# Optimization experiments

Hardware: AMD Instinct MI355X
Metric: run time of the kernel (lower is better)

## Reference

```python
import jax, jax.numpy as jnp
import numpy as np

B, D, H, W, C = 2, 128, 128, 128, 8
GD = GH = GW = 96


def setup_inputs() -> dict:
    key = jax.random.key(0)
    k1, k2 = jax.random.split(key)
    inputs = jax.random.normal(k1, (B, D, H, W, C), dtype=jnp.float32)
    # sample_coords uniform over the valid voxel range [0, size-1] per spatial dim
    sizes = jnp.array([D - 1, H - 1, W - 1], dtype=jnp.float32)
    sample_coords = jax.random.uniform(k2, (B, GD, GH, GW, 3), dtype=jnp.float32) * sizes
    return {"inputs": inputs, "sample_coords": sample_coords}


def reference(inputs, sample_coords):
    # Trilinear resampling with REPLICATE boundary (clamp), matching
    # ResamplerLayer.resample_linear + boundary_replicate.
    input_size = inputs.shape[1:-1]                       # (D, H, W)
    rank = len(input_size)                                # 3
    floor_c = jnp.floor(sample_coords)                    # [B, gd, gh, gw, 3]
    w = sample_coords - floor_c                           # fractional weights
    wc = 1.0 - w
    i0 = floor_c.astype(jnp.int32)
    c0 = [jnp.clip(i0[..., d], 0, input_size[d] - 1) for d in range(rank)]
    c1 = [jnp.clip(i0[..., d] + 1, 0, input_size[d] - 1) for d in range(rank)]

    bsz = sample_coords.shape[0]
    batch_idx = jnp.arange(bsz).reshape((bsz,) + (1,) * (sample_coords.ndim - 2))

    # Sum over the 2^rank corners; identical math to the recursive
    # pyramid_combination in the original (fixed small unrolled loop).
    out = jnp.zeros(sample_coords.shape[:-1] + (inputs.shape[-1],), inputs.dtype)
    for code in range(2 ** rank):
        bits = [(code >> (rank - 1 - d)) & 1 for d in range(rank)]
        idx = [c1[d] if bits[d] else c0[d] for d in range(rank)]
        samp = inputs[batch_idx, idx[0], idx[1], idx[2]]  # [B, gd, gh, gw, C]
        wt = jnp.ones(sample_coords.shape[:-1], inputs.dtype)
        for d in range(rank):
            wt = wt * (w[..., d] if bits[d] else wc[..., d])
        out = out + samp * wt[..., None]
    return out
```

## Files before the change

kernel.cpp:

```cpp
#include <hip/hip_runtime.h>
#include <stdint.h>


constexpr int B  = 2;
constexpr int D  = 128;
constexpr int H  = 128;
constexpr int W  = 128;
constexpr int C  = 8;
constexpr int GD = 96;
constexpr int GH = 96;
constexpr int GW = 96;
constexpr long long PTS_PER_B = (long long)GD * GH * GW;
constexpr long long NPTS      = (long long)B * PTS_PER_B;
constexpr int NPTS_I = (int)NPTS;

constexpr int TPZ = 16, TPY = 16, TPX = 8;
constexpr int NT_PER_B = TPZ * TPY * TPX;
constexpr int NT = B * NT_PER_B;

constexpr int RZ = 9, RY = 9, RX = 17;
constexpr int RVOX = RZ * RY * RX;

constexpr int TPB_BIN = 1024;
constexpr int PPT     = 8;
constexpr int NB_BIN  = NPTS_I / (TPB_BIN * PPT);
static_assert(NB_BIN * TPB_BIN * PPT == NPTS_I, "exact tiling");
constexpr int BPT = NT / TPB_BIN;

__device__ __forceinline__ int clampi(int v, int lo, int hi) {
    return min(max(v, lo), hi);
}

__device__ __forceinline__ unsigned long long
pack_rec(int i, float zc, float yc, float xc, int b, int& tk)
{
    const int z0 = clampi((int)floorf(zc), 0, D - 1);
    const int y0 = clampi((int)floorf(yc), 0, H - 1);
    const int x0 = clampi((int)floorf(xc), 0, W - 1);
    const int tz = z0 >> 3, ty = y0 >> 3, tx = x0 >> 4;
    tk = (b << 11) | (tz << 7) | (ty << 3) | tx;
    const int qz = clampi((int)((zc - (float)(tz << 3)) * 1024.0f + 0.5f), 0,  8191);
    const int qy = clampi((int)((yc - (float)(ty << 3)) * 1024.0f + 0.5f), 0,  8191);
    const int qx = clampi((int)((xc - (float)(tx << 4)) * 1024.0f + 0.5f), 0, 16383);
    return (unsigned long long)(uint32_t)i
         | ((unsigned long long)qx << 21)
         | ((unsigned long long)qy << 35)
         | ((unsigned long long)qz << 48);
}

__device__ __forceinline__ int tile_of(int b, float zc, float yc, float xc) {
    int z0 = clampi((int)floorf(zc), 0, D - 1);
    int y0 = clampi((int)floorf(yc), 0, H - 1);
    int x0 = clampi((int)floorf(xc), 0, W - 1);
    return (b << 11) | ((z0 >> 3) << 7) | ((y0 >> 3) << 3) | (x0 >> 4);
}

__device__ __forceinline__ uint32_t bf16_rne(float f) {
    uint32_t u = __float_as_uint(f);
    u += 0x7FFFu + ((u >> 16) & 1u);
    return u >> 16;
}
__device__ __forceinline__ uint32_t pack_bf16(float lo, float hi) {
    return bf16_rne(lo) | (bf16_rne(hi) << 16);
}

__global__ __launch_bounds__(TPB_BIN)
void k_hist(const float* __restrict__ coords, uint16_t* __restrict__ blockHist)
{
    __shared__ uint32_t h[NT];
    const int t = threadIdx.x;
#pragma unroll
    for (int j = 0; j < BPT; ++j) h[t + j * TPB_BIN] = 0u;
    __syncthreads();

    const int base = blockIdx.x * (TPB_BIN * PPT);
#pragma unroll
    for (int k = 0; k < PPT; ++k) {
        const int i = base + k * TPB_BIN + t;
        const float zc = coords[3 * i + 0];
        const float yc = coords[3 * i + 1];
        const float xc = coords[3 * i + 2];
        const int b = (i >= (int)PTS_PER_B) ? 1 : 0;
        atomicAdd(&h[tile_of(b, zc, yc, xc)], 1u);
    }
    __syncthreads();
#pragma unroll
    for (int j = 0; j < BPT; ++j) {
        const int c = t + j * TPB_BIN;
        blockHist[blockIdx.x * NT + c] = (uint16_t)h[c];
    }
}

__global__ __launch_bounds__(128)
void k_scan_cols(uint16_t* __restrict__ blockHist, uint32_t* __restrict__ bucketTot)
{
    const int c = blockIdx.x * 128 + threadIdx.x;
    uint32_t acc = 0u;
#pragma unroll 8
    for (int r = 0; r < NB_BIN; ++r) {
        const int o = r * NT + c;
        const uint32_t v = blockHist[o];
        blockHist[o] = (uint16_t)acc;
        acc += v;
    }
    bucketTot[c] = acc;
}

__global__ __launch_bounds__(TPB_BIN)
void k_scan_base(const uint32_t* __restrict__ bucketTot, uint32_t* __restrict__ bucketBase)
{
    __shared__ uint32_t ss[TPB_BIN];
    const int t = threadIdx.x;

    uint32_t l[BPT];
    uint32_t ls = 0u;
#pragma unroll
    for (int j = 0; j < BPT; ++j) {
        l[j] = bucketTot[t * BPT + j];
        ls += l[j];
    }
    ss[t] = ls;
    __syncthreads();
    for (int off = 1; off < TPB_BIN; off <<= 1) {
        const uint32_t v = (t >= off) ? ss[t - off] : 0u;
        __syncthreads();
        ss[t] += v;
        __syncthreads();
    }
    uint32_t basev = ss[t] - ls;
#pragma unroll
    for (int j = 0; j < BPT; ++j) {
        bucketBase[t * BPT + j] = basev;
        basev += l[j];
    }
    if (t == TPB_BIN - 1) bucketBase[NT] = (uint32_t)NPTS_I;
}

__global__ __launch_bounds__(TPB_BIN)
void k_scatter(const float* __restrict__ coords,
               const uint16_t* __restrict__ blockHist,
               const uint32_t* __restrict__ bucketBase,
               unsigned long long* __restrict__ records)
{
    __shared__ uint32_t cur[NT];
    const int t = threadIdx.x;
#pragma unroll
    for (int j = 0; j < BPT; ++j) {
        const int c = t + j * TPB_BIN;
        cur[c] = (uint32_t)blockHist[blockIdx.x * NT + c] + bucketBase[c];
    }
    __syncthreads();

    const int base = blockIdx.x * (TPB_BIN * PPT);
#pragma unroll
    for (int k = 0; k < PPT; ++k) {
        const int i = base + k * TPB_BIN + t;
        const float zc = coords[3 * i + 0];
        const float yc = coords[3 * i + 1];
        const float xc = coords[3 * i + 2];
        const int b = (i >= (int)PTS_PER_B) ? 1 : 0;
        int tk;
        const unsigned long long r = pack_rec(i, zc, yc, xc, b, tk);
        const uint32_t slot = atomicAdd(&cur[tk], 1u);
        records[slot] = r;
    }
}

__device__ __forceinline__ void
process_rec(unsigned long long r, const uint4* __restrict__ tb,
            float* __restrict__ out)
{
    const int idx = (int)(r & 0x1FFFFFull);
    const int qx  = (int)((r >> 21) & 0x3FFFull);
    const int qy  = (int)((r >> 35) & 0x1FFFull);
    const int qz  = (int)((r >> 48) & 0x1FFFull);
    const int lx = qx >> 10, ly = qy >> 10, lz = qz >> 10;
    const float wx1 = (float)(qx & 1023) * (1.0f / 1024.0f), wx0 = 1.0f - wx1;
    const float wy1 = (float)(qy & 1023) * (1.0f / 1024.0f), wy0 = 1.0f - wy1;
    const float wz1 = (float)(qz & 1023) * (1.0f / 1024.0f), wz0 = 1.0f - wz1;

    const int vi = (lz * RY + ly) * RX + lx;

    float a0 = 0.f, a1 = 0.f, a2 = 0.f, a3 = 0.f;
    float a4 = 0.f, a5 = 0.f, a6 = 0.f, a7 = 0.f;
    const float wzs[2] = {wz0, wz1};
    const float wys[2] = {wy0, wy1};
    const float wxs[2] = {wx0, wx1};

#pragma unroll
    for (int iz = 0; iz < 2; ++iz) {
#pragma unroll
        for (int iy = 0; iy < 2; ++iy) {
#pragma unroll
            for (int ix = 0; ix < 2; ++ix) {
                const float wt = wzs[iz] * wys[iy] * wxs[ix];
                const int cv = vi + (iz * RY + iy) * RX + ix;
                const uint4 rv = tb[cv];
                a0 += wt * __uint_as_float(rv.x << 16);
                a1 += wt * __uint_as_float(rv.x & 0xFFFF0000u);
                a2 += wt * __uint_as_float(rv.y << 16);
                a3 += wt * __uint_as_float(rv.y & 0xFFFF0000u);
                a4 += wt * __uint_as_float(rv.z << 16);
                a5 += wt * __uint_as_float(rv.z & 0xFFFF0000u);
                a6 += wt * __uint_as_float(rv.w << 16);
                a7 += wt * __uint_as_float(rv.w & 0xFFFF0000u);
            }
        }
    }

    float* o = out + (long long)idx * C;
    *reinterpret_cast<float4*>(o)     = make_float4(a0, a1, a2, a3);
    *reinterpret_cast<float4*>(o + 4) = make_float4(a4, a5, a6, a7);
}

__global__ __launch_bounds__(256)
void k_sample_tiled(const float* __restrict__ inp,
                    const unsigned long long* __restrict__ records,
                    const uint32_t* __restrict__ bucketBase,
                    float* __restrict__ out)
{
    __shared__ uint4 tile[RVOX];
    const int t = threadIdx.x;

    const int g = blockIdx.x;
    const int c = (g & 7) * (NT >> 3) + (g >> 3);

    const int tx = c & 7;
    const int ty = (c >> 3) & 15;
    const int tz = (c >> 7) & 15;
    const int b  = c >> 11;
    const int z0r = tz << 3, y0r = ty << 3, x0r = tx << 4;

    const uint32_t s = bucketBase[c];
    const uint32_t e = bucketBase[c + 1];
    const bool v0 = (s + (uint32_t)t        < e);
    const bool v1 = (s + (uint32_t)t + 256u < e);
    unsigned long long r0 = 0ull, r1 = 0ull;
    if (v0) r0 = records[s + (uint32_t)t];
    if (v1) r1 = records[s + (uint32_t)t + 256u];

#pragma unroll
    for (int half = 0; half < 2; ++half) {
        float4 a0[3], a1[3];
#pragma unroll
        for (int j = 0; j < 3; ++j) {
            const int v = t + (half * 3 + j) * 256;
            if (v < RVOX) {
                const int lz = v / (RY * RX);
                const int rr = v - lz * (RY * RX);
                const int ly = rr / RX;
                const int lx = rr - ly * RX;
                const int gz = min(z0r + lz, D - 1);
                const int gy = min(y0r + ly, H - 1);
                const int gx = min(x0r + lx, W - 1);
                const int a = ((((b << 7) | gz) << 7 | gy) << 7 | gx) * C;
                a0[j] = *reinterpret_cast<const float4*>(inp + a);
                a1[j] = *reinterpret_cast<const float4*>(inp + a + 4);
            }
        }
#pragma unroll
        for (int j = 0; j < 3; ++j) {
            const int v = t + (half * 3 + j) * 256;
            if (v < RVOX) {
                uint4 pk;
                pk.x = pack_bf16(a0[j].x, a0[j].y);
                pk.y = pack_bf16(a0[j].z, a0[j].w);
                pk.z = pack_bf16(a1[j].x, a1[j].y);
                pk.w = pack_bf16(a1[j].z, a1[j].w);
                tile[v] = pk;
            }
        }
    }
    __syncthreads();

    if (v0) process_rec(r0, tile, out);
    if (v1) process_rec(r1, tile, out);
    for (uint32_t i = s + (uint32_t)t + 512u; i < e; i += 256u)
        process_rec(records[i], tile, out);
}

__global__ __launch_bounds__(256)
void resample_direct(const float* __restrict__ inp,
                     const float* __restrict__ coords,
                     float* __restrict__ out)
{
    const long long i = (long long)blockIdx.x * blockDim.x + threadIdx.x;
    if (i >= NPTS) return;
    const int b = (i >= PTS_PER_B) ? 1 : 0;
    const float zc = coords[3 * i + 0];
    const float yc = coords[3 * i + 1];
    const float xc = coords[3 * i + 2];
    const float fz = floorf(zc), fy = floorf(yc), fx = floorf(xc);
    const float wz1 = zc - fz, wz0 = 1.0f - wz1;
    const float wy1 = yc - fy, wy0 = 1.0f - wy1;
    const float wx1 = xc - fx, wx0 = 1.0f - wx1;
    const int z0 = clampi((int)fz, 0, D - 1);
    const int y0 = clampi((int)fy, 0, H - 1);
    const int x0 = clampi((int)fx, 0, W - 1);
    const int z1 = min(z0 + 1, D - 1);
    const int y1 = min(y0 + 1, H - 1);
    const int x1 = min(x0 + 1, W - 1);
    float4 acc_lo = make_float4(0.f, 0.f, 0.f, 0.f);
    float4 acc_hi = make_float4(0.f, 0.f, 0.f, 0.f);
    const int   zs[2]  = {z0, z1};
    const int   ys[2]  = {y0, y1};
    const int   xs[2]  = {x0, x1};
    const float wzs[2] = {wz0, wz1};
    const float wys[2] = {wy0, wy1};
    const float wxs[2] = {wx0, wx1};
#pragma unroll
    for (int iz = 0; iz < 2; ++iz)
#pragma unroll
        for (int iy = 0; iy < 2; ++iy)
#pragma unroll
            for (int ix = 0; ix < 2; ++ix) {
                const float wt = wzs[iz] * wys[iy] * wxs[ix];
                const int base = ((((b << 7) | zs[iz]) << 7 | ys[iy]) << 7 | xs[ix]) * C;
                const float4 v0 = *reinterpret_cast<const float4*>(inp + base);
                const float4 v1 = *reinterpret_cast<const float4*>(inp + base + 4);
                acc_lo.x += wt * v0.x;  acc_lo.y += wt * v0.y;
                acc_lo.z += wt * v0.z;  acc_lo.w += wt * v0.w;
                acc_hi.x += wt * v1.x;  acc_hi.y += wt * v1.y;
                acc_hi.z += wt * v1.z;  acc_hi.w += wt * v1.w;
            }
    float* o = out + i * C;
    *reinterpret_cast<float4*>(o)     = acc_lo;
    *reinterpret_cast<float4*>(o + 4) = acc_hi;
}

extern "C" void kernel_launch(void* const* d_in, const int* in_sizes, int n_in,
                              void* d_out, int out_size, void* d_ws, size_t ws_size,
                              hipStream_t stream)
{
    const float* inp    = (const float*)d_in[0];
    const float* coords = (const float*)d_in[1];
    float* out          = (float*)d_out;

    const size_t rec_bytes  = (size_t)NPTS_I * sizeof(unsigned long long);
    const size_t hist_bytes = (size_t)NB_BIN * NT * sizeof(uint16_t);
    const size_t base_bytes = (size_t)(NT + 1) * sizeof(uint32_t);
    const size_t tot_bytes  = (size_t)NT * sizeof(uint32_t);
    const size_t needed     = rec_bytes + hist_bytes + base_bytes + tot_bytes;

    if (ws_size < needed) {
        const int nblk = (NPTS_I + 255) / 256;
        resample_direct<<<nblk, 256, 0, stream>>>(inp, coords, out);
        return;
    }

    unsigned long long* records = (unsigned long long*)d_ws;
    uint16_t* blockHist  = (uint16_t*)((char*)d_ws + rec_bytes);
    uint32_t* bucketBase = (uint32_t*)((char*)d_ws + rec_bytes + hist_bytes);
    uint32_t* bucketTot  = (uint32_t*)((char*)d_ws + rec_bytes + hist_bytes + base_bytes);

    k_hist        <<<NB_BIN,   TPB_BIN, 0, stream>>>(coords, blockHist);
    k_scan_cols   <<<NT / 128, 128,     0, stream>>>(blockHist, bucketTot);
    k_scan_base   <<<1,        TPB_BIN, 0, stream>>>(bucketTot, bucketBase);
    k_scatter     <<<NB_BIN,   TPB_BIN, 0, stream>>>(coords, blockHist, bucketBase, records);
    k_sample_tiled<<<NT,       256,     0, stream>>>(inp, records, bucketBase, out);
}
```

Before: 86.96 us.

## Shrink LDS tile z-halo to 8 slices, fetch upper-z corners from global

The shared-memory tile drops its ninth z-slice, so each block stages 8x9x17 voxels instead of 9x9x17. Samples whose upper z corner falls outside the tile (lz==7 in non-top tiles) read those four corners straight from global memory in fp32. The aim is less staging traffic and LDS footprint per block, which may raise occupancy. The cost is divergent global gathers for about one eighth of the samples, and those corners now use fp32 instead of bf16 values.

```diff
diff --git a/kernel.cpp b/kernel.cpp
--- a/kernel.cpp
+++ b/kernel.cpp
@@ -18,8 +18,8 @@
 constexpr int NT_PER_B = TPZ * TPY * TPX;
 constexpr int NT = B * NT_PER_B;
 
-constexpr int RZ = 9, RY = 9, RX = 17;
-constexpr int RVOX = RZ * RY * RX;
+constexpr int SRZ = 8, RY = 9, RX = 17;
+constexpr int RVOX = SRZ * RY * RX;
 
 constexpr int TPB_BIN = 1024;
 constexpr int PPT     = 8;
@@ -166,53 +166,6 @@
     }
 }
 
-__device__ __forceinline__ void
-process_rec(unsigned long long r, const uint4* __restrict__ tb,
-            float* __restrict__ out)
-{
-    const int idx = (int)(r & 0x1FFFFFull);
-    const int qx  = (int)((r >> 21) & 0x3FFFull);
-    const int qy  = (int)((r >> 35) & 0x1FFFull);
-    const int qz  = (int)((r >> 48) & 0x1FFFull);
-    const int lx = qx >> 10, ly = qy >> 10, lz = qz >> 10;
-    const float wx1 = (float)(qx & 1023) * (1.0f / 1024.0f), wx0 = 1.0f - wx1;
-    const float wy1 = (float)(qy & 1023) * (1.0f / 1024.0f), wy0 = 1.0f - wy1;
-    const float wz1 = (float)(qz & 1023) * (1.0f / 1024.0f), wz0 = 1.0f - wz1;
-
-    const int vi = (lz * RY + ly) * RX + lx;
-
-    float a0 = 0.f, a1 = 0.f, a2 = 0.f, a3 = 0.f;
-    float a4 = 0.f, a5 = 0.f, a6 = 0.f, a7 = 0.f;
-    const float wzs[2] = {wz0, wz1};
-    const float wys[2] = {wy0, wy1};
-    const float wxs[2] = {wx0, wx1};
-
-#pragma unroll
-    for (int iz = 0; iz < 2; ++iz) {
-#pragma unroll
-        for (int iy = 0; iy < 2; ++iy) {
-#pragma unroll
-            for (int ix = 0; ix < 2; ++ix) {
-                const float wt = wzs[iz] * wys[iy] * wxs[ix];
-                const int cv = vi + (iz * RY + iy) * RX + ix;
-                const uint4 rv = tb[cv];
-                a0 += wt * __uint_as_float(rv.x << 16);
-                a1 += wt * __uint_as_float(rv.x & 0xFFFF0000u);
-                a2 += wt * __uint_as_float(rv.y << 16);
-                a3 += wt * __uint_as_float(rv.y & 0xFFFF0000u);
-                a4 += wt * __uint_as_float(rv.z << 16);
-                a5 += wt * __uint_as_float(rv.z & 0xFFFF0000u);
-                a6 += wt * __uint_as_float(rv.w << 16);
-                a7 += wt * __uint_as_float(rv.w & 0xFFFF0000u);
-            }
-        }
-    }
-
-    float* o = out + (long long)idx * C;
-    *reinterpret_cast<float4*>(o)     = make_float4(a0, a1, a2, a3);
-    *reinterpret_cast<float4*>(o + 4) = make_float4(a4, a5, a6, a7);
-}
-
 __global__ __launch_bounds__(256)
 void k_sample_tiled(const float* __restrict__ inp,
                     const unsigned long long* __restrict__ records,
@@ -230,53 +183,143 @@
     const int tz = (c >> 7) & 15;
     const int b  = c >> 11;
     const int z0r = tz << 3, y0r = ty << 3, x0r = tx << 4;
+    const bool top_tile = (tz == 15);
+    const int zpart = ((b << 7) | (z0r + 8)) << 14;
 
     const uint32_t s = bucketBase[c];
     const uint32_t e = bucketBase[c + 1];
-    const bool v0 = (s + (uint32_t)t        < e);
-    const bool v1 = (s + (uint32_t)t + 256u < e);
+    const bool rv0 = (s + (uint32_t)t        < e);
+    const bool rv1 = (s + (uint32_t)t + 256u < e);
     unsigned long long r0 = 0ull, r1 = 0ull;
-    if (v0) r0 = records[s + (uint32_t)t];
-    if (v1) r1 = records[s + (uint32_t)t + 256u];
-
-#pragma unroll
-    for (int half = 0; half < 2; ++half) {
+    if (rv0) r0 = records[s + (uint32_t)t];
+    if (rv1) r1 = records[s + (uint32_t)t + 256u];
+
+    {
         float4 a0[3], a1[3];
 #pragma unroll
         for (int j = 0; j < 3; ++j) {
-            const int v = t + (half * 3 + j) * 256;
+            const int v = t + j * 256;
+            const int lz = v / (RY * RX);
+            const int rr = v - lz * (RY * RX);
+            const int ly = rr / RX;
+            const int lx = rr - ly * RX;
+            const int gy = min(y0r + ly, H - 1);
+            const int gx = min(x0r + lx, W - 1);
+            const int a = ((((b << 7) | (z0r + lz)) << 7 | gy) << 7 | gx) * C;
+            a0[j] = *reinterpret_cast<const float4*>(inp + a);
+            a1[j] = *reinterpret_cast<const float4*>(inp + a + 4);
+        }
+#pragma unroll
+        for (int j = 0; j < 3; ++j) {
+            const int v = t + j * 256;
+            uint4 pk;
+            pk.x = pack_bf16(a0[j].x, a0[j].y);
+            pk.y = pack_bf16(a0[j].z, a0[j].w);
+            pk.z = pack_bf16(a1[j].x, a1[j].y);
+            pk.w = pack_bf16(a1[j].z, a1[j].w);
+            tile[v] = pk;
+        }
+#pragma unroll
+        for (int j = 3; j < 5; ++j) {
+            const int v = t + j * 256;
             if (v < RVOX) {
                 const int lz = v / (RY * RX);
                 const int rr = v - lz * (RY * RX);
                 const int ly = rr / RX;
                 const int lx = rr - ly * RX;
-                const int gz = min(z0r + lz, D - 1);
                 const int gy = min(y0r + ly, H - 1);
                 const int gx = min(x0r + lx, W - 1);
-                const int a = ((((b << 7) | gz) << 7 | gy) << 7 | gx) * C;
-                a0[j] = *reinterpret_cast<const float4*>(inp + a);
-                a1[j] = *reinterpret_cast<const float4*>(inp + a + 4);
+                const int a = ((((b << 7) | (z0r + lz)) << 7 | gy) << 7 | gx) * C;
+                a0[j - 3] = *reinterpret_cast<const float4*>(inp + a);
+                a1[j - 3] = *reinterpret_cast<const float4*>(inp + a + 4);
             }
         }
 #pragma unroll
-        for (int j = 0; j < 3; ++j) {
-            const int v = t + (half * 3 + j) * 256;
+        for (int j = 3; j < 5; ++j) {
+            const int v = t + j * 256;
             if (v < RVOX) {
                 uint4 pk;
-                pk.x = pack_bf16(a0[j].x, a0[j].y);
-                pk.y = pack_bf16(a0[j].z, a0[j].w);
-                pk.z = pack_bf16(a1[j].x, a1[j].y);
-                pk.w = pack_bf16(a1[j].z, a1[j].w);
+                pk.x = pack_bf16(a0[j - 3].x, a0[j - 3].y);
+                pk.y = pack_bf16(a0[j - 3].z, a0[j - 3].w);
+                pk.z = pack_bf16(a1[j - 3].x, a1[j - 3].y);
+                pk.w = pack_bf16(a1[j - 3].z, a1[j - 3].w);
                 tile[v] = pk;
             }
         }
     }
     __syncthreads();
 
-    if (v0) process_rec(r0, tile, out);
-    if (v1) process_rec(r1, tile, out);
+    auto sample = [&](unsigned long long r) {
+        const int idx = (int)(r & 0x1FFFFFull);
+        const int qx  = (int)((r >> 21) & 0x3FFFull);
+        const int qy  = (int)((r >> 35) & 0x1FFFull);
+        const int qz  = (int)((r >> 48) & 0x1FFFull);
+        const int lx = qx >> 10, ly = qy >> 10, lz = qz >> 10;
+        const float wx1 = (float)(qx & 1023) * (1.0f / 1024.0f), wx0 = 1.0f - wx1;
+        const float wy1 = (float)(qy & 1023) * (1.0f / 1024.0f), wy0 = 1.0f - wy1;
+        const float wz1 = (float)(qz & 1023) * (1.0f / 1024.0f), wz0 = 1.0f - wz1;
+
+        const float wys[2] = {wy0, wy1};
+        const float wxs[2] = {wx0, wx1};
+
+        float a0 = 0.f, a1 = 0.f, a2 = 0.f, a3 = 0.f;
+        float a4 = 0.f, a5 = 0.f, a6 = 0.f, a7 = 0.f;
+
+        auto lds_corner = [&](int cv, float wt) {
+            const uint4 rv = tile[cv];
+            a0 += wt * __uint_as_float(rv.x << 16);
+            a1 += wt * __uint_as_float(rv.x & 0xFFFF0000u);
+            a2 += wt * __uint_as_float(rv.y << 16);
+            a3 += wt * __uint_as_float(rv.y & 0xFFFF0000u);
+            a4 += wt * __uint_as_float(rv.z << 16);
+            a5 += wt * __uint_as_float(rv.z & 0xFFFF0000u);
+            a6 += wt * __uint_as_float(rv.w << 16);
+            a7 += wt * __uint_as_float(rv.w & 0xFFFF0000u);
+        };
+
+        const int vlo = (lz * RY + ly) * RX + lx;
+#pragma unroll
+        for (int iy = 0; iy < 2; ++iy)
+#pragma unroll
+            for (int ix = 0; ix < 2; ++ix)
+                lds_corner(vlo + iy * RX + ix, wz0 * wys[iy] * wxs[ix]);
+
+        const int zhi = (lz < 7) ? (lz + 1) : (top_tile ? 7 : -1);
+        if (zhi >= 0) {
+            const int vhi = (zhi * RY + ly) * RX + lx;
+#pragma unroll
+            for (int iy = 0; iy < 2; ++iy)
+#pragma unroll
+                for (int ix = 0; ix < 2; ++ix)
+                    lds_corner(vhi + iy * RX + ix, wz1 * wys[iy] * wxs[ix]);
+        } else {
+#pragma unroll
+            for (int iy = 0; iy < 2; ++iy) {
+#pragma unroll
+                for (int ix = 0; ix < 2; ++ix) {
+                    const float wt = wz1 * wys[iy] * wxs[ix];
+                    const int gy = min(y0r + ly + iy, H - 1);
+                    const int gx = min(x0r + lx + ix, W - 1);
+                    const int a = (zpart | (gy << 7) | gx) * C;
+                    const float4 v0 = *reinterpret_cast<const float4*>(inp + a);
+                    const float4 v1 = *reinterpret_cast<const float4*>(inp + a + 4);
+                    a0 += wt * v0.x;  a1 += wt * v0.y;
+                    a2 += wt * v0.z;  a3 += wt * v0.w;
+                    a4 += wt * v1.x;  a5 += wt * v1.y;
+                    a6 += wt * v1.z;  a7 += wt * v1.w;
+                }
+            }
+        }
+
+        float* o = out + (long long)idx * C;
+        *reinterpret_cast<float4*>(o)     = make_float4(a0, a1, a2, a3);
+        *reinterpret_cast<float4*>(o + 4) = make_float4(a4, a5, a6, a7);
+    };
+
+    if (rv0) sample(r0);
+    if (rv1) sample(r1);
     for (uint32_t i = s + (uint32_t)t + 512u; i < e; i += 256u)
-        process_rec(records[i], tile, out);
+        sample(records[i]);
 }
 
 __global__ __launch_bounds__(256)
```

New measurement: 87.49 us. About the same (+0.6%).

## Shrink sampling tiles to 4x8x8 and give each wavefront its own tile

Applied to the files above, without the earlier changes.

Binning tiles shrink from 8x8x16 to 4x8x8 voxels, which quadruples the number of buckets. The sampling kernel now assigns one tile per 64-lane wavefront, with four private LDS tiles per 256-thread block. Each wave synchronizes with an lgkmcnt wait instead of a block-wide __syncthreads, and prefetches the next record while sampling the current one. The aim is to remove block-level barriers and improve load balance. The cost is a larger per-tile halo overhead and a per-block histogram and scan workspace that grows with the bucket count.

```diff
diff --git a/kernel.cpp b/kernel.cpp
--- a/kernel.cpp
+++ b/kernel.cpp
@@ -14,11 +14,11 @@
 constexpr long long NPTS      = (long long)B * PTS_PER_B;
 constexpr int NPTS_I = (int)NPTS;
 
-constexpr int TPZ = 16, TPY = 16, TPX = 8;
+constexpr int TPZ = 32, TPY = 16, TPX = 16;
 constexpr int NT_PER_B = TPZ * TPY * TPX;
 constexpr int NT = B * NT_PER_B;
 
-constexpr int RZ = 9, RY = 9, RX = 17;
+constexpr int RZ = 5, RY = 9, RX = 9;
 constexpr int RVOX = RZ * RY * RX;
 
 constexpr int TPB_BIN = 1024;
@@ -27,32 +27,35 @@
 static_assert(NB_BIN * TPB_BIN * PPT == NPTS_I, "exact tiling");
 constexpr int BPT = NT / TPB_BIN;
 
+constexpr int WPB  = 4;
+constexpr int NBLK = NT / WPB;
+
 __device__ __forceinline__ int clampi(int v, int lo, int hi) {
     return min(max(v, lo), hi);
-}
-
-__device__ __forceinline__ unsigned long long
-pack_rec(int i, float zc, float yc, float xc, int b, int& tk)
-{
-    const int z0 = clampi((int)floorf(zc), 0, D - 1);
-    const int y0 = clampi((int)floorf(yc), 0, H - 1);
-    const int x0 = clampi((int)floorf(xc), 0, W - 1);
-    const int tz = z0 >> 3, ty = y0 >> 3, tx = x0 >> 4;
-    tk = (b << 11) | (tz << 7) | (ty << 3) | tx;
-    const int qz = clampi((int)((zc - (float)(tz << 3)) * 1024.0f + 0.5f), 0,  8191);
-    const int qy = clampi((int)((yc - (float)(ty << 3)) * 1024.0f + 0.5f), 0,  8191);
-    const int qx = clampi((int)((xc - (float)(tx << 4)) * 1024.0f + 0.5f), 0, 16383);
-    return (unsigned long long)(uint32_t)i
-         | ((unsigned long long)qx << 21)
-         | ((unsigned long long)qy << 35)
-         | ((unsigned long long)qz << 48);
 }
 
 __device__ __forceinline__ int tile_of(int b, float zc, float yc, float xc) {
     int z0 = clampi((int)floorf(zc), 0, D - 1);
     int y0 = clampi((int)floorf(yc), 0, H - 1);
     int x0 = clampi((int)floorf(xc), 0, W - 1);
-    return (b << 11) | ((z0 >> 3) << 7) | ((y0 >> 3) << 3) | (x0 >> 4);
+    return (b << 13) | ((z0 >> 2) << 8) | ((y0 >> 3) << 4) | (x0 >> 3);
+}
+
+__device__ __forceinline__ unsigned long long
+pack_rec(int i, float zc, float yc, float xc, int b, int& tk)
+{
+    const int z0 = clampi((int)floorf(zc), 0, D - 1);
+    const int y0 = clampi((int)floorf(yc), 0, H - 1);
+    const int x0 = clampi((int)floorf(xc), 0, W - 1);
+    const int tz = z0 >> 2, ty = y0 >> 3, tx = x0 >> 3;
+    tk = (b << 13) | (tz << 8) | (ty << 4) | tx;
+    const int qz = clampi((int)((zc - (float)(tz << 2)) * 1024.0f + 0.5f), 0, 4095);
+    const int qy = clampi((int)((yc - (float)(ty << 3)) * 1024.0f + 0.5f), 0, 8191);
+    const int qx = clampi((int)((xc - (float)(tx << 3)) * 1024.0f + 0.5f), 0, 8191);
+    return (unsigned long long)(uint32_t)i
+         | ((unsigned long long)qx << 21)
+         | ((unsigned long long)qy << 34)
+         | ((unsigned long long)qz << 47);
 }
 
 __device__ __forceinline__ uint32_t bf16_rne(float f) {
@@ -166,85 +169,64 @@
     }
 }
 
-__device__ __forceinline__ void
-process_rec(unsigned long long r, const uint4* __restrict__ tb,
-            float* __restrict__ out)
-{
-    const int idx = (int)(r & 0x1FFFFFull);
-    const int qx  = (int)((r >> 21) & 0x3FFFull);
-    const int qy  = (int)((r >> 35) & 0x1FFFull);
-    const int qz  = (int)((r >> 48) & 0x1FFFull);
-    const int lx = qx >> 10, ly = qy >> 10, lz = qz >> 10;
-    const float wx1 = (float)(qx & 1023) * (1.0f / 1024.0f), wx0 = 1.0f - wx1;
-    const float wy1 = (float)(qy & 1023) * (1.0f / 1024.0f), wy0 = 1.0f - wy1;
-    const float wz1 = (float)(qz & 1023) * (1.0f / 1024.0f), wz0 = 1.0f - wz1;
-
-    const int vi = (lz * RY + ly) * RX + lx;
-
-    float a0 = 0.f, a1 = 0.f, a2 = 0.f, a3 = 0.f;
-    float a4 = 0.f, a5 = 0.f, a6 = 0.f, a7 = 0.f;
-    const float wzs[2] = {wz0, wz1};
-    const float wys[2] = {wy0, wy1};
-    const float wxs[2] = {wx0, wx1};
-
-#pragma unroll
-    for (int iz = 0; iz < 2; ++iz) {
-#pragma unroll
-        for (int iy = 0; iy < 2; ++iy) {
-#pragma unroll
-            for (int ix = 0; ix < 2; ++ix) {
-                const float wt = wzs[iz] * wys[iy] * wxs[ix];
-                const int cv = vi + (iz * RY + iy) * RX + ix;
-                const uint4 rv = tb[cv];
-                a0 += wt * __uint_as_float(rv.x << 16);
-                a1 += wt * __uint_as_float(rv.x & 0xFFFF0000u);
-                a2 += wt * __uint_as_float(rv.y << 16);
-                a3 += wt * __uint_as_float(rv.y & 0xFFFF0000u);
-                a4 += wt * __uint_as_float(rv.z << 16);
-                a5 += wt * __uint_as_float(rv.z & 0xFFFF0000u);
-                a6 += wt * __uint_as_float(rv.w << 16);
-                a7 += wt * __uint_as_float(rv.w & 0xFFFF0000u);
-            }
-        }
-    }
-
-    float* o = out + (long long)idx * C;
-    *reinterpret_cast<float4*>(o)     = make_float4(a0, a1, a2, a3);
-    *reinterpret_cast<float4*>(o + 4) = make_float4(a4, a5, a6, a7);
-}
-
 __global__ __launch_bounds__(256)
-void k_sample_tiled(const float* __restrict__ inp,
-                    const unsigned long long* __restrict__ records,
-                    const uint32_t* __restrict__ bucketBase,
-                    float* __restrict__ out)
-{
-    __shared__ uint4 tile[RVOX];
-    const int t = threadIdx.x;
-
-    const int g = blockIdx.x;
-    const int c = (g & 7) * (NT >> 3) + (g >> 3);
-
-    const int tx = c & 7;
-    const int ty = (c >> 3) & 15;
-    const int tz = (c >> 7) & 15;
-    const int b  = c >> 11;
-    const int z0r = tz << 3, y0r = ty << 3, x0r = tx << 4;
+void k_sample_wave(const float* __restrict__ inp,
+                   const unsigned long long* __restrict__ records,
+                   const uint32_t* __restrict__ bucketBase,
+                   float* __restrict__ out)
+{
+    __shared__ uint4 tile[WPB][RVOX];
+    const int t    = threadIdx.x;
+    const int w    = t >> 6;
+    const int lane = t & 63;
+
+    const int g  = blockIdx.x;
+    const int gb = (g & 7) * (NBLK >> 3) + (g >> 3);
+    const int c  = gb * WPB + w;
+
+    const int tx = c & 15;
+    const int ty = (c >> 4) & 15;
+    const int tz = (c >> 8) & 31;
+    const int b  = c >> 13;
+    const int z0r = tz << 2, y0r = ty << 3, x0r = tx << 3;
+
+    uint4* tb = tile[w];
 
     const uint32_t s = bucketBase[c];
     const uint32_t e = bucketBase[c + 1];
-    const bool v0 = (s + (uint32_t)t        < e);
-    const bool v1 = (s + (uint32_t)t + 256u < e);
-    unsigned long long r0 = 0ull, r1 = 0ull;
-    if (v0) r0 = records[s + (uint32_t)t];
-    if (v1) r1 = records[s + (uint32_t)t + 256u];
-
-#pragma unroll
-    for (int half = 0; half < 2; ++half) {
-        float4 a0[3], a1[3];
-#pragma unroll
-        for (int j = 0; j < 3; ++j) {
-            const int v = t + (half * 3 + j) * 256;
+    const bool rv0 = (s + (uint32_t)lane < e);
+    unsigned long long r0 = 0ull;
+    if (rv0) r0 = records[s + (uint32_t)lane];
+
+    {
+        float4 a0[4], a1[4];
+#pragma unroll
+        for (int j = 0; j < 4; ++j) {
+            const int v = lane + j * 64;
+            const int lz = v / (RY * RX);
+            const int rr = v - lz * (RY * RX);
+            const int ly = rr / RX;
+            const int lx = rr - ly * RX;
+            const int gz = min(z0r + lz, D - 1);
+            const int gy = min(y0r + ly, H - 1);
+            const int gx = min(x0r + lx, W - 1);
+            const int a = ((((b << 7) | gz) << 7 | gy) << 7 | gx) * C;
+            a0[j] = *reinterpret_cast<const float4*>(inp + a);
+            a1[j] = *reinterpret_cast<const float4*>(inp + a + 4);
+        }
+#pragma unroll
+        for (int j = 0; j < 4; ++j) {
+            const int v = lane + j * 64;
+            uint4 pk;
+            pk.x = pack_bf16(a0[j].x, a0[j].y);
+            pk.y = pack_bf16(a0[j].z, a0[j].w);
+            pk.z = pack_bf16(a1[j].x, a1[j].y);
+            pk.w = pack_bf16(a1[j].z, a1[j].w);
+            tb[v] = pk;
+        }
+#pragma unroll
+        for (int j = 4; j < 7; ++j) {
+            const int v = lane + j * 64;
             if (v < RVOX) {
                 const int lz = v / (RY * RX);
                 const int rr = v - lz * (RY * RX);
@@ -254,29 +236,81 @@
                 const int gy = min(y0r + ly, H - 1);
                 const int gx = min(x0r + lx, W - 1);
                 const int a = ((((b << 7) | gz) << 7 | gy) << 7 | gx) * C;
-                a0[j] = *reinterpret_cast<const float4*>(inp + a);
-                a1[j] = *reinterpret_cast<const float4*>(inp + a + 4);
+                a0[j - 4] = *reinterpret_cast<const float4*>(inp + a);
+                a1[j - 4] = *reinterpret_cast<const float4*>(inp + a + 4);
             }
         }
 #pragma unroll
-        for (int j = 0; j < 3; ++j) {
-            const int v = t + (half * 3 + j) * 256;
+        for (int j = 4; j < 7; ++j) {
+            const int v = lane + j * 64;
             if (v < RVOX) {
                 uint4 pk;
-                pk.x = pack_bf16(a0[j].x, a0[j].y);
-                pk.y = pack_bf16(a0[j].z, a0[j].w);
-                pk.z = pack_bf16(a1[j].x, a1[j].y);
-                pk.w = pack_bf16(a1[j].z, a1[j].w);
-                tile[v] = pk;
+                pk.x = pack_bf16(a0[j - 4].x, a0[j - 4].y);
+                pk.y = pack_bf16(a0[j - 4].z, a0[j - 4].w);
+                pk.z = pack_bf16(a1[j - 4].x, a1[j - 4].y);
+                pk.w = pack_bf16(a1[j - 4].z, a1[j - 4].w);
+                tb[v] = pk;
             }
         }
     }
-    __syncthreads();
-
-    if (v0) process_rec(r0, tile, out);
-    if (v1) process_rec(r1, tile, out);
-    for (uint32_t i = s + (uint32_t)t + 512u; i < e; i += 256u)
-        process_rec(records[i], tile, out);
+    asm volatile("s_waitcnt lgkmcnt(0)" ::: "memory");
+    __builtin_amdgcn_sched_barrier(0);
+
+    auto sample = [&](unsigned long long r) {
+        const int idx = (int)(r & 0x1FFFFFull);
+        const int qx  = (int)((r >> 21) & 0x1FFFull);
+        const int qy  = (int)((r >> 34) & 0x1FFFull);
+        const int qz  = (int)((r >> 47) & 0x1FFFull);
+        const int lx = qx >> 10, ly = qy >> 10, lz = qz >> 10;
+        const float wx1 = (float)(qx & 1023) * (1.0f / 1024.0f), wx0 = 1.0f - wx1;
+        const float wy1 = (float)(qy & 1023) * (1.0f / 1024.0f), wy0 = 1.0f - wy1;
+        const float wz1 = (float)(qz & 1023) * (1.0f / 1024.0f), wz0 = 1.0f - wz1;
+
+        const int vi = (lz * RY + ly) * RX + lx;
+
+        float a0 = 0.f, a1 = 0.f, a2 = 0.f, a3 = 0.f;
+        float a4 = 0.f, a5 = 0.f, a6 = 0.f, a7 = 0.f;
+        const float wzs[2] = {wz0, wz1};
+        const float wys[2] = {wy0, wy1};
+        const float wxs[2] = {wx0, wx1};
+
+#pragma unroll
+        for (int iz = 0; iz < 2; ++iz) {
+#pragma unroll
+            for (int iy = 0; iy < 2; ++iy) {
+#pragma unroll
+                for (int ix = 0; ix < 2; ++ix) {
+                    const float wt = wzs[iz] * wys[iy] * wxs[ix];
+                    const int cv = vi + (iz * RY + iy) * RX + ix;
+                    const uint4 rv = tb[cv];
+                    a0 += wt * __uint_as_float(rv.x << 16);
+                    a1 += wt * __uint_as_float(rv.x & 0xFFFF0000u);
+                    a2 += wt * __uint_as_float(rv.y << 16);
+                    a3 += wt * __uint_as_float(rv.y & 0xFFFF0000u);
+                    a4 += wt * __uint_as_float(rv.z << 16);
+                    a5 += wt * __uint_as_float(rv.z & 0xFFFF0000u);
+                    a6 += wt * __uint_as_float(rv.w << 16);
+                    a7 += wt * __uint_as_float(rv.w & 0xFFFF0000u);
+                }
+            }
+        }
+
+        float* o = out + (long long)idx * C;
+        *reinterpret_cast<float4*>(o)     = make_float4(a0, a1, a2, a3);
+        *reinterpret_cast<float4*>(o + 4) = make_float4(a4, a5, a6, a7);
+    };
+
+    uint32_t i = s + (uint32_t)lane + 64u;
+    unsigned long long rn = 0ull;
+    if (i < e) rn = records[i];
+    if (rv0) sample(r0);
+    while (i < e) {
+        const unsigned long long rc = rn;
+        const uint32_t inext = i + 64u;
+        if (inext < e) rn = records[inext];
+        sample(rc);
+        i = inext;
+    }
 }
 
 __global__ __launch_bounds__(256)
@@ -353,9 +387,9 @@
     uint32_t* bucketBase = (uint32_t*)((char*)d_ws + rec_bytes + hist_bytes);
     uint32_t* bucketTot  = (uint32_t*)((char*)d_ws + rec_bytes + hist_bytes + base_bytes);
 
-    k_hist        <<<NB_BIN,   TPB_BIN, 0, stream>>>(coords, blockHist);
-    k_scan_cols   <<<NT / 128, 128,     0, stream>>>(blockHist, bucketTot);
-    k_scan_base   <<<1,        TPB_BIN, 0, stream>>>(bucketTot, bucketBase);
-    k_scatter     <<<NB_BIN,   TPB_BIN, 0, stream>>>(coords, blockHist, bucketBase, records);
-    k_sample_tiled<<<NT,       256,     0, stream>>>(inp, records, bucketBase, out);
-}
+    k_hist       <<<NB_BIN,   TPB_BIN, 0, stream>>>(coords, blockHist);
+    k_scan_cols  <<<NT / 128, 128,     0, stream>>>(blockHist, bucketTot);
+    k_scan_base  <<<1,        TPB_BIN, 0, stream>>>(bucketTot, bucketBase);
+    k_scatter    <<<NB_BIN,   TPB_BIN, 0, stream>>>(coords, blockHist, bucketBase, records);
+    k_sample_wave<<<NBLK,     256,     0, stream>>>(inp, records, bucketBase, out);
+}
```

Result: slower. 95.34 us (+9.6%).
